# Kernel optimization log

Hardware: AMD Instinct MI355X
Metric: run time of the kernel (lower is better)

Reference implementation:

```python
import jax, jax.numpy as jnp
import numpy as np
from jax import lax

DN = ('NCHW', 'OIHW', 'NCHW')

def _conv(x, w, b):
    # Conv2d(k=4, stride=2, padding=1): H -> H/2
    y = lax.conv_general_dilated(x, w, (2, 2), ((1, 1), (1, 1)), dimension_numbers=DN)
    return y + b[None, :, None, None]

def _deconv(x, w, b):
    # ConvTranspose2d(k=4, stride=2, padding=1): H -> 2H.
    # Equivalent dense conv: flip kernel spatially, swap in/out channels,
    # lhs_dilation = stride, padding = k-1-p = 2.
    wf = jnp.flip(w, (2, 3)).transpose(1, 0, 2, 3)  # (out, in, 4, 4)
    y = lax.conv_general_dilated(x, wf, (1, 1), ((2, 2), (2, 2)), lhs_dilation=(2, 2), dimension_numbers=DN)
    return y + b[None, :, None, None]

def setup_inputs() -> dict:
    key = jax.random.key(0)
    ks = jax.random.split(key, 20)
    f = jnp.float32
    s = 0.05  # small init scale for stability
    inp = {
        'x':   jax.random.uniform(ks[0], (64, 3, 224, 224), dtype=f),
        # encoder conv weights (OIHW) + biases
        'ew1': jax.random.normal(ks[1], (32, 3, 4, 4), f) * s,   'eb1': jnp.zeros((32,), f),
        'ew2': jax.random.normal(ks[2], (64, 32, 4, 4), f) * s,  'eb2': jnp.zeros((64,), f),
        'ew3': jax.random.normal(ks[3], (128, 64, 4, 4), f) * s, 'eb3': jnp.zeros((128,), f),
        'ew4': jax.random.normal(ks[4], (64, 128, 4, 4), f) * s, 'eb4': jnp.zeros((64,), f),
        # codebook: uniform(-1/K, 1/K) like torch init, K=4000, D=12544
        'emb': jax.random.uniform(ks[5], (4000, 12544), f, -1.0 / 4000, 1.0 / 4000),
        # decoder conv-transpose weights in torch layout (in, out, kh, kw) + biases
        'dw1': jax.random.normal(ks[6], (64, 128, 4, 4), f) * s, 'db1': jnp.zeros((128,), f),
        'dw2': jax.random.normal(ks[7], (128, 64, 4, 4), f) * s, 'db2': jnp.zeros((64,), f),
        'dw3': jax.random.normal(ks[8], (64, 32, 4, 4), f) * s,  'db3': jnp.zeros((32,), f),
        'dw4': jax.random.normal(ks[9], (32, 3, 4, 4), f) * s,   'db4': jnp.zeros((3,), f),
    }
    return inp

def reference(x, ew1, eb1, ew2, eb2, ew3, eb3, ew4, eb4, emb,
              dw1, db1, dw2, db2, dw3, db3, dw4, db4):
    sg = lax.stop_gradient
    B = x.shape[0]
    # ---- Encoder ----
    h = jax.nn.relu(_conv(x, ew1, eb1))
    h = jax.nn.relu(_conv(h, ew2, eb2))
    h = jax.nn.relu(_conv(h, ew3, eb3))
    h = _conv(h, ew4, eb4)                 # (B, 64, 14, 14)
    z = h.reshape(B, -1)                   # (B, 12544)
    # ---- Vector quantization ----
    # ||z||^2 - 2 z E^T + ||e||^2, argmin over codebook
    dist = (jnp.sum(z * z, axis=1, keepdims=True)
            - 2.0 * (z @ emb.T)
            + jnp.sum(emb * emb, axis=1))  # (B, 4000)
    idx = jnp.argmin(dist, axis=1)         # (B,)
    quantized = emb[idx]                   # (B, 12544) -- direct gather (== onehot @ emb)
    e_latent = jnp.mean((sg(quantized) - z) ** 2)
    q_latent = jnp.mean((quantized - sg(z)) ** 2)
    vq_loss = q_latent + 0.25 * e_latent
    zq = z + sg(quantized - z)             # straight-through
    # ---- Decoder ----
    d = zq.reshape(B, 64, 14, 14)
    d = jax.nn.relu(_deconv(d, dw1, db1))
    d = jax.nn.relu(_deconv(d, dw2, db2))
    d = jax.nn.relu(_deconv(d, dw3, db3))
    x_recon = jax.nn.sigmoid(_deconv(d, dw4, db4))  # (B, 3, 224, 224)
    recon_loss = jnp.mean((x_recon - x) ** 2)
    loss = recon_loss + vq_loss
    return (x_recon, loss, recon_loss, vq_loss)
```

## Files before the change

kernel.cpp:

```cpp
#include <hip/hip_runtime.h>
#include <math.h>

typedef unsigned short u16;
typedef unsigned int u32;
typedef __attribute__((ext_vector_type(8))) short short8;
typedef __attribute__((ext_vector_type(4))) float f32x4;

__device__ __forceinline__ u16 f2bf(float f) {
    u32 u = __float_as_uint(f);
    u = u + 0x7fffu + ((u >> 16) & 1u);
    return (u16)(u >> 16);
}
__device__ __forceinline__ float bf2f(u16 h) { return __uint_as_float(((u32)h) << 16); }

__device__ __forceinline__ f32x4 mfma16(short8 a, short8 b, f32x4 c) {
    return __builtin_amdgcn_mfma_f32_16x16x32_bf16(a, b, c, 0, 0, 0);
}

__device__ __forceinline__ uint4 pack8(float4 a, float4 b) {
    uint4 r;
    r.x = (u32)f2bf(a.x) | ((u32)f2bf(a.y) << 16);
    r.y = (u32)f2bf(a.z) | ((u32)f2bf(a.w) << 16);
    r.z = (u32)f2bf(b.x) | ((u32)f2bf(b.y) << 16);
    r.w = (u32)f2bf(b.z) | ((u32)f2bf(b.w) << 16);
    return r;
}

#define GLOAD_LDS16(gsrc, ldst)                                                      \
    __builtin_amdgcn_global_load_lds(                                                \
        (__attribute__((address_space(1))) u32*)(gsrc),                              \
        (__attribute__((address_space(3))) u32*)(ldst), 16, 0, 0)

__device__ __forceinline__ void prep1_item(const float* __restrict__ w,
                                           u16* __restrict__ o, int i)
{
    int j = i & 7; int kx = j >> 1, cp = j & 1;
    int r = i >> 3;
    int co = r & 31; int r2 = r >> 5;
    int ky = r2 & 3; int h = r2 >> 2;
    int ci = 2 * h + cp;
    o[i] = (ci < 3) ? f2bf(w[((co * 3 + ci) * 16) + ky * 4 + kx]) : (u16)0;
}
__device__ __forceinline__ void prepc_item(const float* __restrict__ w,
                                           u16* __restrict__ o, int CIN, int COUT, int i)
{
    int j = i & 7; int r = i >> 3;
    int co = r % COUT; int r2 = r / COUT;
    int tap = r2 & 15; int ch = r2 >> 4;
    int ci = ch * 8 + j;
    o[i] = f2bf(w[((size_t)co * CIN + ci) * 16 + tap]);
}
__device__ __forceinline__ void prepd_item(const float* __restrict__ w,
                                           u16* __restrict__ o, int CIN, int COUT,
                                           int COPAD, int i)
{
    int j = i & 7; int r = i >> 3;
    int co = r % COPAD; int r2 = r / COPAD;
    int t16 = r2 & 15; int ch = r2 >> 4;
    int py = t16 >> 3, px = (t16 >> 2) & 1, qq = t16 & 3;
    int ta = qq >> 1, tb = qq & 1;
    int ky = py + 2 * ta, kx = px + 2 * tb;
    int ci = ch * 8 + j;
    o[i] = (co < COUT) ? f2bf(w[(((size_t)ci * COUT + co) * 16) + ky * 4 + kx]) : (u16)0;
}

__global__ __launch_bounds__(256) void prep_all(
    const float* __restrict__ ew1, const float* __restrict__ ew2,
    const float* __restrict__ ew3, const float* __restrict__ ew4,
    const float* __restrict__ dw1, const float* __restrict__ dw2,
    const float* __restrict__ dw3, const float* __restrict__ dw4,
    u16* __restrict__ w1c, u16* __restrict__ wc2,
    u16* __restrict__ wc3, u16* __restrict__ wc4,
    u16* __restrict__ wd1, u16* __restrict__ wd2,
    u16* __restrict__ wd3, u16* __restrict__ wd4)
{
    int i = blockIdx.x * 256 + threadIdx.x;
    if (i < 2048) { prep1_item(ew1, w1c, i); return; }
    i -= 2048;
    if (i < 32768)  { prepc_item(ew2, wc2, 32, 64, i); return; }
    i -= 32768;
    if (i < 131072) { prepc_item(ew3, wc3, 64, 128, i); return; }
    i -= 131072;
    if (i < 131072) { prepc_item(ew4, wc4, 128, 64, i); return; }
    i -= 131072;
    if (i < 131072) { prepd_item(dw1, wd1, 64, 128, 128, i); return; }
    i -= 131072;
    if (i < 131072) { prepd_item(dw2, wd2, 128, 64, 64, i); return; }
    i -= 131072;
    if (i < 32768)  { prepd_item(dw3, wd3, 64, 32, 32, i); return; }
    i -= 32768;
    if (i < 8192)   { prepd_item(dw4, wd4, 32, 3, 16, i); return; }
}

template<int CIN, int COUT, int COTILE, int H2, int W2, int NSEG, int MB,
         int MBW, int NWF, int RELU, int STOREZ>
__global__ __launch_bounds__(256) void conv_mfma(
    const u16* __restrict__ in, const u16* __restrict__ wcvt,
    const float* __restrict__ bias, u16* __restrict__ outp,
    float* __restrict__ z32)
{
    constexpr int CHUNKS = CIN / 8, CGI = CIN / 8, CGO = COUT / 8;
    constexpr int HIN = H2 * 2, WIN = W2 * 2, SLOTW = 35;
    constexpr int NF = COTILE / 16, WM = MB / MBW, WN = NF / NWF;
    static_assert(WM * WN == 4, "wave layout");
    constexpr int TBu = MB * 4 * SLOTW, WBu = 16 * COTILE;
    constexpr int EBu = (MB * 16 * COTILE * 2 + 15) / 16;
    constexpr int SM = (TBu + WBu) > EBu ? (TBu + WBu) : EBu;
    __shared__ uint4 smem[SM];
    uint4* T = smem; uint4* wS = smem + TBu;
    u16* E = (u16*)smem;

    const int tid = threadIdx.x, wid = tid >> 6, lane = tid & 63;
    const int q = lane >> 4, lm = lane & 15;
    const int wm = wid / WN, wn = wid % WN;
    const int cobase = blockIdx.y * COTILE;
    const int mbase = blockIdx.x * MB;

    f32x4 acc[MBW][NWF];
    #pragma unroll
    for (int a = 0; a < MBW; ++a)
        #pragma unroll
        for (int b = 0; b < NWF; ++b) {
            acc[a][b][0] = 0.f; acc[a][b][1] = 0.f;
            acc[a][b][2] = 0.f; acc[a][b][3] = 0.f;
        }

    for (int ch = 0; ch < CHUNKS; ++ch) {
        __syncthreads();
        for (int ib = 0; ib < TBu; ib += 256) {
            int i = ib + tid;
            uint4* ldst = T + ib + (wid << 6);
            if (i < TBu) {
                int mb = i / (4 * SLOTW), r2 = i % (4 * SLOTW);
                int r = r2 / SLOTW, s = r2 % SLOTW;
                int mbg = mbase + mb;
                int n = mbg / (H2 * NSEG), rr = mbg % (H2 * NSEG);
                int oy = rr / NSEG, ox0 = (rr % NSEG) << 4;
                int iy = 2 * oy - 1 + r, ix = 2 * ox0 - 1 + s;
                if ((unsigned)iy < (unsigned)HIN && (unsigned)ix < (unsigned)WIN) {
                    GLOAD_LDS16(in + (size_t)(((n * CGI + ch) * HIN + iy) * WIN + ix) * 8, ldst);
                } else {
                    uint4 zz = {0u, 0u, 0u, 0u};
                    T[i] = zz;
                }
            }
        }
        for (int ib = 0; ib < WBu; ib += 256) {
            int i = ib + tid;
            int tap = i / COTILE, co = i % COTILE;
            GLOAD_LDS16(wcvt + (size_t)((ch * 16 + tap) * COUT + cobase + co) * 8,
                        wS + ib + (wid << 6));
        }
        __syncthreads();
        #pragma unroll
        for (int ky = 0; ky < 4; ++ky) {
            short8 Af[MBW]; short8 Bf[NWF];
            #pragma unroll
            for (int im = 0; im < MBW; ++im) {
                int mb = wm * MBW + im;
                Af[im] = *(const short8*)(T + (mb * 4 + ky) * SLOTW + 2 * lm + q);
            }
            #pragma unroll
            for (int inf = 0; inf < NWF; ++inf)
                Bf[inf] = *(const short8*)(wS + (ky * 4 + q) * COTILE + wn * NWF * 16 + inf * 16 + lm);
            #pragma unroll
            for (int im = 0; im < MBW; ++im)
                #pragma unroll
                for (int inf = 0; inf < NWF; ++inf)
                    acc[im][inf] = mfma16(Af[im], Bf[inf], acc[im][inf]);
        }
    }
    __syncthreads();
    #pragma unroll
    for (int inf = 0; inf < NWF; ++inf) {
        int col = wn * NWF * 16 + inf * 16 + lm;
        float bv = bias[cobase + col];
        #pragma unroll
        for (int im = 0; im < MBW; ++im) {
            int pixb = (wm * MBW + im) * 16 + q * 4;
            #pragma unroll
            for (int r = 0; r < 4; ++r) {
                float v = acc[im][inf][r] + bv;
                if (RELU) v = fmaxf(v, 0.f);
                E[(pixb + r) * COTILE + col] = f2bf(v);
            }
        }
    }
    __syncthreads();
    for (int i = tid; i < MB * 16 * (COTILE / 8); i += 256) {
        int pix = i / (COTILE / 8), cg = i % (COTILE / 8);
        int mb = pix >> 4, m = pix & 15;
        int mbg = mbase + mb;
        int n = mbg / (H2 * NSEG), rr = mbg % (H2 * NSEG);
        int oy = rr / NSEG, ox0 = (rr % NSEG) << 4;
        int ox = ox0 + m;
        if (ox < W2)
            *(uint4*)(outp + (size_t)(((n * CGO + cobase / 8 + cg) * H2 + oy) * W2 + ox) * 8) =
                *(uint4*)(E + pix * COTILE + cg * 8);
    }
    if (STOREZ) {
        for (int i = tid; i < MB * 16 * COTILE; i += 256) {
            int pix = i / COTILE, co = i % COTILE;
            int mb = pix >> 4, m = pix & 15;
            int mbg = mbase + mb;
            int n = mbg / (H2 * NSEG), rr = mbg % (H2 * NSEG);
            int oy = rr / NSEG, ox0 = (rr % NSEG) << 4;
            int ox = ox0 + m;
            if (ox < W2)
                z32[(size_t)((n * COUT + cobase + co) * H2 + oy) * W2 + ox] =
                    bf2f(E[pix * COTILE + co]);
        }
    }
}

__global__ __launch_bounds__(256) void conv1_mfma(
    const float* __restrict__ x, const u16* __restrict__ w1c,
    const float* __restrict__ bias, u16* __restrict__ outp)
{
    constexpr int MB = 16, MBW = 4, NWF = 2, COTILE = 32, W2 = 112, H2 = 112, NSEG = 7;
    constexpr int TBu = MB * 2 * 64, WBu = 256;
    __shared__ uint4 smem[TBu + WBu];
    uint4* T1 = smem; uint4* w1S = smem + TBu;
    u16* E = (u16*)smem;

    const int tid = threadIdx.x, wid = tid >> 6, lane = tid & 63;
    const int q = lane >> 4, lm = lane & 15;
    const int wm = wid;
    const int mbase = blockIdx.x * MB;

    f32x4 acc[MBW][NWF];
    #pragma unroll
    for (int a = 0; a < MBW; ++a)
        #pragma unroll
        for (int b = 0; b < NWF; ++b) {
            acc[a][b][0] = 0.f; acc[a][b][1] = 0.f;
            acc[a][b][2] = 0.f; acc[a][b][3] = 0.f;
        }

    for (int i = tid; i < TBu; i += 256) {
        int mb = i >> 7; int r = i & 127;
        int h = r >> 6; int r2 = r & 63;
        int ky = r2 >> 4; int m = r2 & 15;
        int mbg = mbase + mb;
        int n = mbg / (H2 * NSEG), rr = mbg % (H2 * NSEG);
        int oy = rr / NSEG, ox0 = (rr % NSEG) << 4;
        int iy = 2 * oy - 1 + ky;
        int ixb = 2 * (ox0 + m) - 1;
        u32 u[4];
        #pragma unroll
        for (int kx = 0; kx < 4; ++kx) {
            float v0 = 0.f, v1 = 0.f;
            int ix = ixb + kx;
            if ((unsigned)iy < 224u && (unsigned)ix < 224u) {
                int ci0 = 2 * h;
                v0 = x[((size_t)(n * 3 + ci0) * 224 + iy) * 224 + ix];
                if (ci0 + 1 < 3) v1 = x[((size_t)(n * 3 + ci0 + 1) * 224 + iy) * 224 + ix];
            }
            u[kx] = (u32)f2bf(v0) | ((u32)f2bf(v1) << 16);
        }
        uint4 vv; vv.x = u[0]; vv.y = u[1]; vv.z = u[2]; vv.w = u[3];
        T1[i] = vv;
    }
    if (tid < 256) {
        w1S[tid] = *(const uint4*)(w1c + (size_t)tid * 8);
    }
    __syncthreads();
    #pragma unroll
    for (int h = 0; h < 2; ++h) {
        short8 Af[MBW]; short8 Bf[NWF];
        #pragma unroll
        for (int im = 0; im < MBW; ++im) {
            int mb = wm * MBW + im;
            Af[im] = *(const short8*)(T1 + (mb * 2 + h) * 64 + lane);
        }
        #pragma unroll
        for (int inf = 0; inf < NWF; ++inf)
            Bf[inf] = *(const short8*)(w1S + (h * 4 + q) * 32 + inf * 16 + lm);
        #pragma unroll
        for (int im = 0; im < MBW; ++im)
            #pragma unroll
            for (int inf = 0; inf < NWF; ++inf)
                acc[im][inf] = mfma16(Af[im], Bf[inf], acc[im][inf]);
    }
    __syncthreads();
    #pragma unroll
    for (int inf = 0; inf < NWF; ++inf) {
        int col = inf * 16 + lm;
        float bv = bias[col];
        #pragma unroll
        for (int im = 0; im < MBW; ++im) {
            int pixb = (wm * MBW + im) * 16 + q * 4;
            #pragma unroll
            for (int r = 0; r < 4; ++r) {
                float v = fmaxf(acc[im][inf][r] + bv, 0.f);
                E[(pixb + r) * COTILE + col] = f2bf(v);
            }
        }
    }
    __syncthreads();
    for (int i = tid; i < MB * 16 * (COTILE / 8); i += 256) {
        int pix = i / (COTILE / 8), cg = i % (COTILE / 8);
        int mb = pix >> 4, m = pix & 15;
        int mbg = mbase + mb;
        int n = mbg / (H2 * NSEG), rr = mbg % (H2 * NSEG);
        int oy = rr / NSEG, ox0 = (rr % NSEG) << 4;
        int ox = ox0 + m;
        *(uint4*)(outp + (size_t)(((n * 4 + cg) * H2 + oy) * W2 + ox) * 8) =
            *(uint4*)(E + pix * COTILE + cg * 8);
    }
}

template<int CIN, int COUT, int COPAD, int COTILE, int Hp, int Wp, int NSEG,
         int MB, int MBW, int NWF, int RELU>
__global__ __launch_bounds__(256) void deconv_mfma(
    const u16* __restrict__ in, const u16* __restrict__ dcvt,
    const float* __restrict__ bias, u16* __restrict__ outp)
{
    constexpr int CHUNKS = CIN / 8, CGI = CIN / 8, CGO = COUT / 8;
    constexpr int SLOTW = 17;
    constexpr int NF = COTILE / 16, WM = MB / MBW, WN = NF / NWF;
    static_assert(WM * WN == 4, "wave layout");
    constexpr int BPP = 64 * Hp * NSEG / MB;
    constexpr int TBu = MB * 2 * SLOTW, WBu = 4 * COTILE;
    constexpr int EBu = (MB * 16 * COTILE * 2 + 15) / 16;
    constexpr int SM = (TBu + WBu) > EBu ? (TBu + WBu) : EBu;
    __shared__ uint4 smem[SM];
    uint4* T = smem; uint4* wS = smem + TBu;
    u16* E = (u16*)smem;

    const int tid = threadIdx.x, wid = tid >> 6, lane = tid & 63;
    const int q = lane >> 4, lm = lane & 15;
    const int wm = wid / WN, wn = wid % WN;
    const int par = blockIdx.x / BPP;
    const int py = par >> 1, px = par & 1;
    const int mbase = (blockIdx.x % BPP) * MB;
    const int cobase = blockIdx.y * COTILE;

    f32x4 acc[MBW][NWF];
    #pragma unroll
    for (int a = 0; a < MBW; ++a)
        #pragma unroll
        for (int b = 0; b < NWF; ++b) {
            acc[a][b][0] = 0.f; acc[a][b][1] = 0.f;
            acc[a][b][2] = 0.f; acc[a][b][3] = 0.f;
        }

    for (int ch = 0; ch < CHUNKS; ++ch) {
        __syncthreads();
        for (int ib = 0; ib < TBu; ib += 256) {
            int i = ib + tid;
            uint4* ldst = T + ib + (wid << 6);
            if (i < TBu) {
                int mb = i / (2 * SLOTW), r2 = i % (2 * SLOTW);
                int rr_ = r2 / SLOTW, s = r2 % SLOTW;
                int mbg = mbase + mb;
                int n = mbg / (Hp * NSEG), rm = mbg % (Hp * NSEG);
                int oyp = rm / NSEG, u0 = (rm % NSEG) << 4;
                int iy = oyp + (1 - py) - 1 + rr_;
                int ix = u0 + (1 - px) - 1 + s;
                if ((unsigned)iy < (unsigned)Hp && (unsigned)ix < (unsigned)Wp) {
                    GLOAD_LDS16(in + (size_t)(((n * CGI + ch) * Hp + iy) * Wp + ix) * 8, ldst);
                } else {
                    uint4 zz = {0u, 0u, 0u, 0u};
                    T[i] = zz;
                }
            }
        }
        for (int ib = 0; ib < WBu; ib += 256) {
            int i = ib + tid;
            if (i < WBu) {
                int qq = i / COTILE, co = i % COTILE;
                GLOAD_LDS16(dcvt + (size_t)((ch * 16 + par * 4 + qq) * COPAD + cobase + co) * 8,
                            wS + ib + (wid << 6));
            }
        }
        __syncthreads();
        {
            short8 Af[MBW]; short8 Bf[NWF];
            #pragma unroll
            for (int im = 0; im < MBW; ++im) {
                int mb = wm * MBW + im;
                Af[im] = *(const short8*)(T + (mb * 2 + (1 - (q >> 1))) * SLOTW + lm + 1 - (q & 1));
            }
            #pragma unroll
            for (int inf = 0; inf < NWF; ++inf)
                Bf[inf] = *(const short8*)(wS + q * COTILE + wn * NWF * 16 + inf * 16 + lm);
            #pragma unroll
            for (int im = 0; im < MBW; ++im)
                #pragma unroll
                for (int inf = 0; inf < NWF; ++inf)
                    acc[im][inf] = mfma16(Af[im], Bf[inf], acc[im][inf]);
        }
    }
    __syncthreads();
    #pragma unroll
    for (int inf = 0; inf < NWF; ++inf) {
        int col = wn * NWF * 16 + inf * 16 + lm;
        float bv = bias[cobase + col];
        #pragma unroll
        for (int im = 0; im < MBW; ++im) {
            int pixb = (wm * MBW + im) * 16 + q * 4;
            #pragma unroll
            for (int r = 0; r < 4; ++r) {
                float v = acc[im][inf][r] + bv;
                if (RELU) v = fmaxf(v, 0.f);
                E[(pixb + r) * COTILE + col] = f2bf(v);
            }
        }
    }
    __syncthreads();
    for (int i = tid; i < MB * 16 * (COTILE / 8); i += 256) {
        int pix = i / (COTILE / 8), cg = i % (COTILE / 8);
        int mb = pix >> 4, m = pix & 15;
        int mbg = mbase + mb;
        int n = mbg / (Hp * NSEG), rm = mbg % (Hp * NSEG);
        int oyp = rm / NSEG, u0 = (rm % NSEG) << 4;
        int u = u0 + m;
        if (u < Wp) {
            int ox = 2 * u + (px ? 0 : 1);
            int oy = 2 * oyp + (py ? 0 : 1);
            *(uint4*)(outp + (size_t)(((n * CGO + cobase / 8 + cg) * (2 * Hp) + oy) * (2 * Wp) + ox) * 8) =
                *(uint4*)(E + pix * COTILE + cg * 8);
        }
    }
}

__global__ __launch_bounds__(256) void deconv4_mfma(
    const u16* __restrict__ in, const u16* __restrict__ dcvt,
    const float* __restrict__ bias, float* __restrict__ outp,
    const float* __restrict__ xref, float* __restrict__ bpart)
{
    constexpr int Hp = 112, Wp = 112, NSEG = 7, MB = 16, MBW = 4;
    constexpr int CGI = 4, CHUNKS = 4;
    constexpr int TROW = 3, TCOL = 18;
    constexpr int TBu = MB * TROW * TCOL;
    __shared__ uint4 smem[TBu + 1024];
    __shared__ float red[4];
    uint4* T = smem; uint4* wS = smem + TBu;
    float* Ef = (float*)smem;

    const int tid = threadIdx.x, wid = tid >> 6, lane = tid & 63;
    const int q = lane >> 4, lm = lane & 15;
    const int wm = wid;
    const int mbase = blockIdx.x * MB;

    f32x4 acc[4][MBW];
    #pragma unroll
    for (int p = 0; p < 4; ++p)
        #pragma unroll
        for (int a = 0; a < MBW; ++a) {
            acc[p][a][0] = 0.f; acc[p][a][1] = 0.f; acc[p][a][2] = 0.f; acc[p][a][3] = 0.f;
        }

    for (int ib = 0; ib < 1024; ib += 256)
        GLOAD_LDS16(dcvt + (size_t)(ib + tid) * 8, wS + ib + (wid << 6));

    for (int ch = 0; ch < CHUNKS; ++ch) {
        __syncthreads();
        for (int ib = 0; ib < TBu; ib += 256) {
            int i = ib + tid;
            uint4* ldst = T + ib + (wid << 6);
            if (i < TBu) {
                int mb = i / (TROW * TCOL), r2 = i % (TROW * TCOL);
                int r = r2 / TCOL, s = r2 % TCOL;
                int mbg = mbase + mb;
                int n = mbg / (Hp * NSEG), rm = mbg % (Hp * NSEG);
                int oyp = rm / NSEG, u0 = (rm % NSEG) << 4;
                int iy = oyp - 1 + r;
                int ix = u0 - 1 + s;
                if ((unsigned)iy < (unsigned)Hp && (unsigned)ix < (unsigned)Wp) {
                    GLOAD_LDS16(in + (size_t)(((n * CGI + ch) * Hp + iy) * Wp + ix) * 8, ldst);
                } else {
                    uint4 zz = {0u, 0u, 0u, 0u};
                    T[i] = zz;
                }
            }
        }
        __syncthreads();
        #pragma unroll
        for (int par = 0; par < 4; ++par) {
            const int py = par >> 1, px = par & 1;
            short8 Bf = *(const short8*)(wS + (ch * 16 + par * 4 + q) * 16 + lm);
            #pragma unroll
            for (int im = 0; im < MBW; ++im) {
                int mb = wm * MBW + im;
                short8 Af = *(const short8*)(T + (mb * TROW + (2 - py - (q >> 1))) * TCOL
                                             + lm + 2 - px - (q & 1));
                acc[par][im] = mfma16(Af, Bf, acc[par][im]);
            }
        }
    }

    __syncthreads();
    if (lm < 3) {
        float bv = bias[lm];
        #pragma unroll
        for (int par = 0; par < 4; ++par)
            #pragma unroll
            for (int im = 0; im < MBW; ++im)
                #pragma unroll
                for (int r = 0; r < 4; ++r)
                    Ef[(((wm * MBW + im) * 16 + q * 4 + r) * 4 + par) * 3 + lm] =
                        acc[par][im][r] + bv;
    }
    __syncthreads();
    float lsum = 0.f;
    #pragma unroll
    for (int k = 0; k < 3; ++k) {
        int i = k * 256 + tid;
        int mb = i / 48, rem = i % 48;
        int row = rem / 24, rem2 = rem % 24;
        int co = rem2 / 8, ox4 = rem2 % 8;
        int mbg = mbase + mb;
        int n = mbg / (Hp * NSEG), rm = mbg % (Hp * NSEG);
        int oyp = rm / NSEG, u0 = (rm % NSEG) << 4;
        int pA = row ? 1 : 3, pB = row ? 0 : 2;
        int uL = 2 * ox4, uH = uL + 1;
        float v0 = Ef[((mb * 16 + uL) * 4 + pA) * 3 + co];
        float v1 = Ef[((mb * 16 + uL) * 4 + pB) * 3 + co];
        float v2 = Ef[((mb * 16 + uH) * 4 + pA) * 3 + co];
        float v3 = Ef[((mb * 16 + uH) * 4 + pB) * 3 + co];
        float4 sv;
        sv.x = 1.f / (1.f + expf(-v0));
        sv.y = 1.f / (1.f + expf(-v1));
        sv.z = 1.f / (1.f + expf(-v2));
        sv.w = 1.f / (1.f + expf(-v3));
        size_t ro = ((size_t)(n * 3 + co) * 224 + 2 * oyp + row) * 224 + 2 * u0 + 4 * ox4;
        float4 x4 = *(const float4*)(xref + ro);
        *(float4*)(outp + ro) = sv;
        float d0 = sv.x - x4.x, d1 = sv.y - x4.y, d2 = sv.z - x4.z, d3 = sv.w - x4.w;
        lsum += d0 * d0 + d1 * d1 + d2 * d2 + d3 * d3;
    }
    #pragma unroll
    for (int off = 32; off > 0; off >>= 1)
        lsum += __shfl_down(lsum, off, 64);
    if (lane == 0) red[wid] = lsum;
    __syncthreads();
    if (tid == 0)
        bpart[blockIdx.x] = red[0] + red[1] + red[2] + red[3];
}

__global__ __launch_bounds__(256) void vq_gemm(
    const float* __restrict__ z32, const float* __restrict__ emb,
    float* __restrict__ P, float* __restrict__ normp)
{
    __shared__ uint4 As[8 * 64];
    __shared__ uint4 Bs[8 * 256];
    const int tid = threadIdx.x, wid = tid >> 6, lane = tid & 63;
    const int q = lane >> 4, lm = lane & 15;
    const int jt = blockIdx.x, ks = blockIdx.y;
    const int jg = jt * 256 + tid;
    const int jc = jg < 4000 ? jg : 3999;
    const float* brow = emb + (size_t)jc * 12544 + ks * 448;
    const int m = tid & 63, ksub = tid >> 6;
    const float* arow = z32 + (size_t)m * 12544 + ks * 448 + ksub * 16;

    f32x4 acc[4][4];
    #pragma unroll
    for (int a = 0; a < 4; ++a)
        #pragma unroll
        for (int b = 0; b < 4; ++b) {
            acc[a][b][0] = 0.f; acc[a][b][1] = 0.f; acc[a][b][2] = 0.f; acc[a][b][3] = 0.f;
        }
    float nsq = 0.f;

    for (int ch = 0; ch < 7; ++ch) {
        __syncthreads();
        {
            float4 f0 = *(const float4*)(arow + ch * 64);
            float4 f1 = *(const float4*)(arow + ch * 64 + 4);
            float4 f2 = *(const float4*)(arow + ch * 64 + 8);
            float4 f3 = *(const float4*)(arow + ch * 64 + 12);
            As[(ksub * 2 + 0) * 64 + m] = pack8(f0, f1);
            As[(ksub * 2 + 1) * 64 + m] = pack8(f2, f3);
        }
        {
            const float* bp = brow + ch * 64;
            #pragma unroll
            for (int ko = 0; ko < 8; ++ko) {
                float4 fa = *(const float4*)(bp + ko * 8);
                float4 fb = *(const float4*)(bp + ko * 8 + 4);
                nsq += fa.x * fa.x + fa.y * fa.y + fa.z * fa.z + fa.w * fa.w
                     + fb.x * fb.x + fb.y * fb.y + fb.z * fb.z + fb.w * fb.w;
                Bs[ko * 256 + tid] = pack8(fa, fb);
            }
        }
        __syncthreads();
        #pragma unroll
        for (int kk = 0; kk < 2; ++kk) {
            short8 Af[4]; short8 Bf[4];
            #pragma unroll
            for (int mf = 0; mf < 4; ++mf)
                Af[mf] = *(const short8*)(As + (kk * 4 + q) * 64 + mf * 16 + lm);
            #pragma unroll
            for (int nf = 0; nf < 4; ++nf)
                Bf[nf] = *(const short8*)(Bs + (kk * 4 + q) * 256 + wid * 64 + nf * 16 + lm);
            #pragma unroll
            for (int mf = 0; mf < 4; ++mf)
                #pragma unroll
                for (int nf = 0; nf < 4; ++nf)
                    acc[mf][nf] = mfma16(Af[mf], Bf[nf], acc[mf][nf]);
        }
    }
    #pragma unroll
    for (int mf = 0; mf < 4; ++mf)
        #pragma unroll
        for (int nf = 0; nf < 4; ++nf) {
            int j = jt * 256 + wid * 64 + nf * 16 + lm;
            if (j < 4000) {
                #pragma unroll
                for (int r = 0; r < 4; ++r) {
                    int b = mf * 16 + q * 4 + r;
                    P[(size_t)(ks * 64 + b) * 4000 + j] = acc[mf][nf][r];
                }
            }
        }
    if (jg < 4000) normp[ks * 4000 + jg] = nsq;
}

__global__ __launch_bounds__(256) void vq_argmin_gather(
    const float* __restrict__ P, const float* __restrict__ normp,
    const float* __restrict__ emb, const float* __restrict__ z32,
    u16* __restrict__ Qb, float* __restrict__ vacc)
{
    const int b = blockIdx.x;
    const int tid = threadIdx.x;
    float best = 3.4e38f;
    int bidx = 0x7fffffff;
    for (int j = tid; j < 4000; j += 256) {
        float dot = 0.f, nrm = 0.f;
        #pragma unroll
        for (int s = 0; s < 28; ++s) {
            dot += P[(size_t)(s * 64 + b) * 4000 + j];
            nrm += normp[s * 4000 + j];
        }
        float d = nrm - 2.f * dot;
        if (d < best) { best = d; bidx = j; }
    }
    __shared__ float sv[256];
    __shared__ int si[256];
    sv[tid] = best; si[tid] = bidx;
    __syncthreads();
    for (int off = 128; off > 0; off >>= 1) {
        if (tid < off) {
            float v2 = sv[tid + off]; int i2 = si[tid + off];
            if (v2 < sv[tid] || (v2 == sv[tid] && i2 < si[tid])) { sv[tid] = v2; si[tid] = i2; }
        }
        __syncthreads();
    }
    const int code = si[0];
    const float* e = emb + (size_t)code * 12544;
    const float* zb = z32 + (size_t)b * 12544;
    float ls = 0.f;
    for (int d = tid; d < 12544; d += 256) {
        float ev = e[d];
        int co = d / 196, rem = d % 196;
        int y = rem / 14, xx = rem % 14;
        Qb[((size_t)((b * 8 + (co >> 3)) * 14 + y) * 14 + xx) * 8 + (co & 7)] = f2bf(ev);
        float df = ev - zb[d];
        ls += df * df;
    }
    #pragma unroll
    for (int off = 32; off > 0; off >>= 1)
        ls += __shfl_down(ls, off, 64);
    if ((tid & 63) == 0) atomicAdd(vacc, ls);
}

__global__ __launch_bounds__(256) void reduce_final(
    const float* __restrict__ bpart, const float* __restrict__ vacc,
    float* __restrict__ tail)
{
    const int tid = threadIdx.x;
    float s = 0.f;
    for (int i = tid; i < 3136; i += 256) s += bpart[i];
    #pragma unroll
    for (int off = 32; off > 0; off >>= 1)
        s += __shfl_down(s, off, 64);
    __shared__ float red[4];
    if ((tid & 63) == 0) red[tid >> 6] = s;
    __syncthreads();
    if (tid == 0) {
        float rsum = red[0] + red[1] + red[2] + red[3];
        float recon = rsum * (1.f / 9633792.f);
        float vq = 1.25f * vacc[0] * (1.f / 802816.f);
        tail[0] = recon + vq;
        tail[1] = recon;
        tail[2] = vq;
    }
}

extern "C" void kernel_launch(void* const* d_in, const int* in_sizes, int n_in,
                              void* d_out, int out_size, void* d_ws, size_t ws_size,
                              hipStream_t stream)
{
    const float* x   = (const float*)d_in[0];
    const float* ew1 = (const float*)d_in[1];
    const float* eb1 = (const float*)d_in[2];
    const float* ew2 = (const float*)d_in[3];
    const float* eb2 = (const float*)d_in[4];
    const float* ew3 = (const float*)d_in[5];
    const float* eb3 = (const float*)d_in[6];
    const float* ew4 = (const float*)d_in[7];
    const float* eb4 = (const float*)d_in[8];
    const float* emb = (const float*)d_in[9];
    const float* dw1 = (const float*)d_in[10];
    const float* db1 = (const float*)d_in[11];
    const float* dw2 = (const float*)d_in[12];
    const float* db2 = (const float*)d_in[13];
    const float* dw3 = (const float*)d_in[14];
    const float* db3 = (const float*)d_in[15];
    const float* dw4 = (const float*)d_in[16];
    const float* db4 = (const float*)d_in[17];
    float* out = (float*)d_out;

    size_t off = 0;
    char* base = (char*)d_ws;
    auto nxt = [&](size_t bytes) -> char* {
        char* p = base + off;
        off = (off + bytes + 255) & ~(size_t)255;
        return p;
    };
    u16*   A1    = (u16*)nxt(25690112ull * 2);
    u16*   A2    = (u16*)nxt(12845056ull * 2);
    u16*   A3    = (u16*)nxt(6422528ull * 2);
    float* z32   = (float*)nxt(802816ull * 4);
    u16*   Qb    = (u16*)nxt(802816ull * 2);
    float* P     = (float*)nxt(28ull * 64 * 4000 * 4);
    float* normp = (float*)nxt(28ull * 4000 * 4);
    u16*   w1c   = (u16*)nxt(2048ull * 2);
    u16*   wc2   = (u16*)nxt(32768ull * 2);
    u16*   wc3   = (u16*)nxt(131072ull * 2);
    u16*   wc4   = (u16*)nxt(131072ull * 2);
    u16*   wd1   = (u16*)nxt(131072ull * 2);
    u16*   wd2   = (u16*)nxt(131072ull * 2);
    u16*   wd3   = (u16*)nxt(32768ull * 2);
    u16*   wd4   = (u16*)nxt(8192ull * 2);
    float* accp  = (float*)nxt(512);
    float* bpart = (float*)nxt(3136ull * 4);
    u16*   D1 = A3;
    u16*   D2 = A2;
    u16*   D3 = A1;

    hipMemsetAsync(accp, 0, 8, stream);

    prep_all<<<2344, 256, 0, stream>>>(ew1, ew2, ew3, ew4, dw1, dw2, dw3, dw4,
                                       w1c, wc2, wc3, wc4, wd1, wd2, wd3, wd4);

    conv1_mfma<<<3136, 256, 0, stream>>>(x, w1c, eb1, A1);
    conv_mfma<32, 64, 64, 56, 56, 4, 16, 8, 2, 1, 0>
        <<<dim3(896, 1), 256, 0, stream>>>(A1, wc2, eb2, A2, nullptr);
    conv_mfma<64, 128, 64, 28, 28, 2, 8, 4, 2, 1, 0>
        <<<dim3(448, 2), 256, 0, stream>>>(A2, wc3, eb3, A3, nullptr);
    conv_mfma<128, 64, 64, 14, 14, 1, 4, 2, 2, 0, 1>
        <<<dim3(224, 1), 256, 0, stream>>>(A3, wc4, eb4, Qb, z32);

    vq_gemm<<<dim3(16, 28), 256, 0, stream>>>(z32, emb, P, normp);
    vq_argmin_gather<<<64, 256, 0, stream>>>(P, normp, emb, z32, Qb, accp);

    deconv_mfma<64, 128, 128, 64, 14, 14, 1, 8, 4, 2, 1>
        <<<dim3(448, 2), 256, 0, stream>>>(Qb, wd1, db1, D1);
    deconv_mfma<128, 64, 64, 64, 28, 28, 2, 16, 8, 2, 1>
        <<<dim3(896, 1), 256, 0, stream>>>(D1, wd2, db2, D2);
    deconv_mfma<64, 32, 32, 32, 56, 56, 4, 16, 8, 1, 1>
        <<<dim3(3584, 1), 256, 0, stream>>>(D2, wd3, db3, D3);
    deconv4_mfma<<<3136, 256, 0, stream>>>(D3, wd4, db4, out, x, bpart);

    reduce_final<<<1, 256, 0, stream>>>(bpart, accp, out + 9633792);
}
```

Measured before the change: 690.4 us.

## Double-buffer LDS staging in conv4/deconv kernels and pre-convert input to bf16

Adds double-buffered shared-memory staging to the last encoder conv and all three mid deconv kernels. The next channel chunk's global-to-LDS loads are issued while MFMAs run on the current chunk, which also removes one barrier per chunk. Separately, a new kernel converts the fp32 input into packed bf16 channel pairs, so conv1 does fewer, wider loads instead of scattered fp32 loads with conversion. The cost is twice the LDS per block, which may lower occupancy, plus an extra pass over the input.

Result: faster. 671.5 us (-2.7%).

```diff
diff --git a/kernel.cpp b/kernel.cpp
--- a/kernel.cpp
+++ b/kernel.cpp
@@ -90,6 +90,21 @@
     if (i < 32768)  { prepd_item(dw3, wd3, 64, 32, 32, i); return; }
     i -= 32768;
     if (i < 8192)   { prepd_item(dw4, wd4, 32, 3, 16, i); return; }
+}
+
+__global__ __launch_bounds__(256) void x2bf(
+    const float* __restrict__ x, u32* __restrict__ xb)
+{
+    const size_t PL = 224 * 224;
+    const size_t TOT = 64 * PL;
+    size_t stride = (size_t)gridDim.x * 256;
+    for (size_t i = (size_t)blockIdx.x * 256 + threadIdx.x; i < TOT; i += stride) {
+        size_t n = i / PL, p = i % PL;
+        const float* xp = x + n * 3 * PL + p;
+        float c0 = xp[0], c1 = xp[PL], c2 = xp[2 * PL];
+        xb[(n * 2 + 0) * PL + p] = (u32)f2bf(c0) | ((u32)f2bf(c1) << 16);
+        xb[(n * 2 + 1) * PL + p] = (u32)f2bf(c2);
+    }
 }
 
 template<int CIN, int COUT, int COTILE, int H2, int W2, int NSEG, int MB,
@@ -213,8 +228,138 @@
     }
 }
 
+template<int CIN, int COUT, int COTILE, int H2, int W2, int NSEG, int MB,
+         int MBW, int NWF, int RELU, int STOREZ>
+__global__ __launch_bounds__(256) void conv_mfma_pf(
+    const u16* __restrict__ in, const u16* __restrict__ wcvt,
+    const float* __restrict__ bias, u16* __restrict__ outp,
+    float* __restrict__ z32)
+{
+    constexpr int CHUNKS = CIN / 8, CGI = CIN / 8, CGO = COUT / 8;
+    constexpr int HIN = H2 * 2, WIN = W2 * 2, SLOTW = 35;
+    constexpr int NF = COTILE / 16, WM = MB / MBW, WN = NF / NWF;
+    static_assert(WM * WN == 4, "wave layout");
+    constexpr int TBu = MB * 4 * SLOTW, WBu = 16 * COTILE;
+    constexpr int BUF = TBu + WBu;
+    constexpr int EBu = (MB * 16 * COTILE * 2 + 15) / 16;
+    constexpr int SM = (2 * BUF) > EBu ? (2 * BUF) : EBu;
+    __shared__ uint4 smem[SM];
+    u16* E = (u16*)smem;
+
+    const int tid = threadIdx.x, wid = tid >> 6, lane = tid & 63;
+    const int q = lane >> 4, lm = lane & 15;
+    const int wm = wid / WN, wn = wid % WN;
+    const int cobase = blockIdx.y * COTILE;
+    const int mbase = blockIdx.x * MB;
+
+    f32x4 acc[MBW][NWF];
+    #pragma unroll
+    for (int a = 0; a < MBW; ++a)
+        #pragma unroll
+        for (int b = 0; b < NWF; ++b) {
+            acc[a][b][0] = 0.f; acc[a][b][1] = 0.f;
+            acc[a][b][2] = 0.f; acc[a][b][3] = 0.f;
+        }
+
+    auto stage = [&](int ch, uint4* buf) {
+        uint4* T = buf; uint4* wS = buf + TBu;
+        for (int ib = 0; ib < TBu; ib += 256) {
+            int i = ib + tid;
+            uint4* ldst = T + ib + (wid << 6);
+            if (i < TBu) {
+                int mb = i / (4 * SLOTW), r2 = i % (4 * SLOTW);
+                int r = r2 / SLOTW, s = r2 % SLOTW;
+                int mbg = mbase + mb;
+                int n = mbg / (H2 * NSEG), rr = mbg % (H2 * NSEG);
+                int oy = rr / NSEG, ox0 = (rr % NSEG) << 4;
+                int iy = 2 * oy - 1 + r, ix = 2 * ox0 - 1 + s;
+                if ((unsigned)iy < (unsigned)HIN && (unsigned)ix < (unsigned)WIN) {
+                    GLOAD_LDS16(in + (size_t)(((n * CGI + ch) * HIN + iy) * WIN + ix) * 8, ldst);
+                } else {
+                    uint4 zz = {0u, 0u, 0u, 0u};
+                    T[i] = zz;
+                }
+            }
+        }
+        for (int ib = 0; ib < WBu; ib += 256) {
+            int i = ib + tid;
+            int tap = i / COTILE, co = i % COTILE;
+            GLOAD_LDS16(wcvt + (size_t)((ch * 16 + tap) * COUT + cobase + co) * 8,
+                        wS + ib + (wid << 6));
+        }
+    };
+
+    uint4* cur = smem;
+    uint4* nxt = smem + BUF;
+    stage(0, cur);
+    __syncthreads();
+    for (int ch = 0; ch < CHUNKS; ++ch) {
+        if (ch + 1 < CHUNKS) stage(ch + 1, nxt);
+        uint4* T = cur; uint4* wS = cur + TBu;
+        #pragma unroll
+        for (int ky = 0; ky < 4; ++ky) {
+            short8 Af[MBW]; short8 Bf[NWF];
+            #pragma unroll
+            for (int im = 0; im < MBW; ++im) {
+                int mb = wm * MBW + im;
+                Af[im] = *(const short8*)(T + (mb * 4 + ky) * SLOTW + 2 * lm + q);
+            }
+            #pragma unroll
+            for (int inf = 0; inf < NWF; ++inf)
+                Bf[inf] = *(const short8*)(wS + (ky * 4 + q) * COTILE + wn * NWF * 16 + inf * 16 + lm);
+            #pragma unroll
+            for (int im = 0; im < MBW; ++im)
+                #pragma unroll
+                for (int inf = 0; inf < NWF; ++inf)
+                    acc[im][inf] = mfma16(Af[im], Bf[inf], acc[im][inf]);
+        }
+        __syncthreads();
+        uint4* t = cur; cur = nxt; nxt = t;
+    }
+    #pragma unroll
+    for (int inf = 0; inf < NWF; ++inf) {
+        int col = wn * NWF * 16 + inf * 16 + lm;
+        float bv = bias[cobase + col];
+        #pragma unroll
+        for (int im = 0; im < MBW; ++im) {
+            int pixb = (wm * MBW + im) * 16 + q * 4;
+            #pragma unroll
+            for (int r = 0; r < 4; ++r) {
+                float v = acc[im][inf][r] + bv;
+                if (RELU) v = fmaxf(v, 0.f);
+                E[(pixb + r) * COTILE + col] = f2bf(v);
+            }
+        }
+    }
+    __syncthreads();
+    for (int i = tid; i < MB * 16 * (COTILE / 8); i += 256) {
+        int pix = i / (COTILE / 8), cg = i % (COTILE / 8);
+        int mb = pix >> 4, m = pix & 15;
+        int mbg = mbase + mb;
+        int n = mbg / (H2 * NSEG), rr = mbg % (H2 * NSEG);
+        int oy = rr / NSEG, ox0 = (rr % NSEG) << 4;
+        int ox = ox0 + m;
+        if (ox < W2)
+            *(uint4*)(outp + (size_t)(((n * CGO + cobase / 8 + cg) * H2 + oy) * W2 + ox) * 8) =
+                *(uint4*)(E + pix * COTILE + cg * 8);
+    }
+    if (STOREZ) {
+        for (int i = tid; i < MB * 16 * COTILE; i += 256) {
+            int pix = i / COTILE, co = i % COTILE;
+            int mb = pix >> 4, m = pix & 15;
+            int mbg = mbase + mb;
+            int n = mbg / (H2 * NSEG), rr = mbg % (H2 * NSEG);
+            int oy = rr / NSEG, ox0 = (rr % NSEG) << 4;
+            int ox = ox0 + m;
+            if (ox < W2)
+                z32[(size_t)((n * COUT + cobase + co) * H2 + oy) * W2 + ox] =
+                    bf2f(E[pix * COTILE + co]);
+        }
+    }
+}
+
 __global__ __launch_bounds__(256) void conv1_mfma(
-    const float* __restrict__ x, const u16* __restrict__ w1c,
+    const u32* __restrict__ xb, const u16* __restrict__ w1c,
     const float* __restrict__ bias, u16* __restrict__ outp)
 {
     constexpr int MB = 16, MBW = 4, NWF = 2, COTILE = 32, W2 = 112, H2 = 112, NSEG = 7;
@@ -246,19 +391,13 @@
         int oy = rr / NSEG, ox0 = (rr % NSEG) << 4;
         int iy = 2 * oy - 1 + ky;
         int ixb = 2 * (ox0 + m) - 1;
-        u32 u[4];
-        #pragma unroll
-        for (int kx = 0; kx < 4; ++kx) {
-            float v0 = 0.f, v1 = 0.f;
-            int ix = ixb + kx;
-            if ((unsigned)iy < 224u && (unsigned)ix < 224u) {
-                int ci0 = 2 * h;
-                v0 = x[((size_t)(n * 3 + ci0) * 224 + iy) * 224 + ix];
-                if (ci0 + 1 < 3) v1 = x[((size_t)(n * 3 + ci0 + 1) * 224 + iy) * 224 + ix];
-            }
-            u[kx] = (u32)f2bf(v0) | ((u32)f2bf(v1) << 16);
-        }
-        uint4 vv; vv.x = u[0]; vv.y = u[1]; vv.z = u[2]; vv.w = u[3];
+        const u32* rowp = xb + ((size_t)(n * 2 + h) * 224 + iy) * 224;
+        bool rok = (unsigned)iy < 224u;
+        uint4 vv;
+        vv.x = (rok && (unsigned)(ixb + 0) < 224u) ? rowp[ixb + 0] : 0u;
+        vv.y = (rok && (unsigned)(ixb + 1) < 224u) ? rowp[ixb + 1] : 0u;
+        vv.z = (rok && (unsigned)(ixb + 2) < 224u) ? rowp[ixb + 2] : 0u;
+        vv.w = (rok && (unsigned)(ixb + 3) < 224u) ? rowp[ixb + 3] : 0u;
         T1[i] = vv;
     }
     if (tid < 256) {
@@ -312,7 +451,7 @@
 
 template<int CIN, int COUT, int COPAD, int COTILE, int Hp, int Wp, int NSEG,
          int MB, int MBW, int NWF, int RELU>
-__global__ __launch_bounds__(256) void deconv_mfma(
+__global__ __launch_bounds__(256) void deconv_mfma_pf(
     const u16* __restrict__ in, const u16* __restrict__ dcvt,
     const float* __restrict__ bias, u16* __restrict__ outp)
 {
@@ -322,10 +461,10 @@
     static_assert(WM * WN == 4, "wave layout");
     constexpr int BPP = 64 * Hp * NSEG / MB;
     constexpr int TBu = MB * 2 * SLOTW, WBu = 4 * COTILE;
+    constexpr int BUF = TBu + WBu;
     constexpr int EBu = (MB * 16 * COTILE * 2 + 15) / 16;
-    constexpr int SM = (TBu + WBu) > EBu ? (TBu + WBu) : EBu;
+    constexpr int SM = (2 * BUF) > EBu ? (2 * BUF) : EBu;
     __shared__ uint4 smem[SM];
-    uint4* T = smem; uint4* wS = smem + TBu;
     u16* E = (u16*)smem;
 
     const int tid = threadIdx.x, wid = tid >> 6, lane = tid & 63;
@@ -345,8 +484,8 @@
             acc[a][b][2] = 0.f; acc[a][b][3] = 0.f;
         }
 
-    for (int ch = 0; ch < CHUNKS; ++ch) {
-        __syncthreads();
+    auto stage = [&](int ch, uint4* buf) {
+        uint4* T = buf; uint4* wS = buf + TBu;
         for (int ib = 0; ib < TBu; ib += 256) {
             int i = ib + tid;
             uint4* ldst = T + ib + (wid << 6);
@@ -374,7 +513,15 @@
                             wS + ib + (wid << 6));
             }
         }
-        __syncthreads();
+    };
+
+    uint4* cur = smem;
+    uint4* nxt = smem + BUF;
+    stage(0, cur);
+    __syncthreads();
+    for (int ch = 0; ch < CHUNKS; ++ch) {
+        if (ch + 1 < CHUNKS) stage(ch + 1, nxt);
+        uint4* T = cur; uint4* wS = cur + TBu;
         {
             short8 Af[MBW]; short8 Bf[NWF];
             #pragma unroll
@@ -391,8 +538,9 @@
                 for (int inf = 0; inf < NWF; ++inf)
                     acc[im][inf] = mfma16(Af[im], Bf[inf], acc[im][inf]);
         }
-    }
-    __syncthreads();
+        __syncthreads();
+        uint4* t = cur; cur = nxt; nxt = t;
+    }
     #pragma unroll
     for (int inf = 0; inf < NWF; ++inf) {
         int col = wn * NWF * 16 + inf * 16 + lm;
@@ -727,6 +875,7 @@
     u16*   Qb    = (u16*)nxt(802816ull * 2);
     float* P     = (float*)nxt(28ull * 64 * 4000 * 4);
     float* normp = (float*)nxt(28ull * 4000 * 4);
+    u32*   xb    = (u32*)nxt(64ull * 2 * 224 * 224 * 4);
     u16*   w1c   = (u16*)nxt(2048ull * 2);
     u16*   wc2   = (u16*)nxt(32768ull * 2);
     u16*   wc3   = (u16*)nxt(131072ull * 2);
@@ -745,23 +894,24 @@
 
     prep_all<<<2344, 256, 0, stream>>>(ew1, ew2, ew3, ew4, dw1, dw2, dw3, dw4,
                                        w1c, wc2, wc3, wc4, wd1, wd2, wd3, wd4);
-
-    conv1_mfma<<<3136, 256, 0, stream>>>(x, w1c, eb1, A1);
+    x2bf<<<2048, 256, 0, stream>>>(x, xb);
+
+    conv1_mfma<<<3136, 256, 0, stream>>>(xb, w1c, eb1, A1);
     conv_mfma<32, 64, 64, 56, 56, 4, 16, 8, 2, 1, 0>
         <<<dim3(896, 1), 256, 0, stream>>>(A1, wc2, eb2, A2, nullptr);
     conv_mfma<64, 128, 64, 28, 28, 2, 8, 4, 2, 1, 0>
         <<<dim3(448, 2), 256, 0, stream>>>(A2, wc3, eb3, A3, nullptr);
-    conv_mfma<128, 64, 64, 14, 14, 1, 4, 2, 2, 0, 1>
+    conv_mfma_pf<128, 64, 64, 14, 14, 1, 4, 2, 2, 0, 1>
         <<<dim3(224, 1), 256, 0, stream>>>(A3, wc4, eb4, Qb, z32);
 
     vq_gemm<<<dim3(16, 28), 256, 0, stream>>>(z32, emb, P, normp);
     vq_argmin_gather<<<64, 256, 0, stream>>>(P, normp, emb, z32, Qb, accp);
 
-    deconv_mfma<64, 128, 128, 64, 14, 14, 1, 8, 4, 2, 1>
+    deconv_mfma_pf<64, 128, 128, 64, 14, 14, 1, 8, 4, 2, 1>
         <<<dim3(448, 2), 256, 0, stream>>>(Qb, wd1, db1, D1);
-    deconv_mfma<128, 64, 64, 64, 28, 28, 2, 16, 8, 2, 1>
+    deconv_mfma_pf<128, 64, 64, 64, 28, 28, 2, 16, 8, 2, 1>
         <<<dim3(896, 1), 256, 0, stream>>>(D1, wd2, db2, D2);
-    deconv_mfma<64, 32, 32, 32, 56, 56, 4, 16, 8, 1, 1>
+    deconv_mfma_pf<64, 32, 32, 32, 56, 56, 4, 16, 8, 1, 1>
         <<<dim3(3584, 1), 256, 0, stream>>>(D2, wd3, db3, D3);
     deconv4_mfma<<<3136, 256, 0, stream>>>(D3, wd4, db4, out, x, bpart);
 
```
